# Kernel tuning notes

Hardware: AMD Instinct MI355X
Metric: run time of the kernel (lower is better)

Reference implementation:

```python
import jax, jax.numpy as jnp
import numpy as np


def log_g(x):
    # log of g(x) = where(x>=0, x+0.5, sigmoid(x)), computed stably in log space
    return jnp.where(x >= 0, jnp.log(jax.nn.relu(x) + 0.5), -jax.nn.softplus(-x))


def setup_inputs() -> dict:
    key = jax.random.key(0)
    k1, k2 = jax.random.split(key)
    B, S, D = 4, 4096, 1024
    x = jax.random.normal(k1, (B, S, D), dtype=jnp.float32)
    W_hg = jax.random.normal(k2, (2 * D, D), dtype=jnp.float32) * (1.0 / np.sqrt(D))
    return {"x": x, "W_hg": W_hg}


def reference(x, W_hg):
    # x: [B, S, D], W_hg: [2D, D]
    hg = jnp.einsum('bsd,ed->bse', x, W_hg)  # [B, S, 2D]
    hidden, gate = jnp.split(hg, 2, axis=-1)

    log_coeffs = -jax.nn.softplus(gate)       # log(1 - z)
    log_z = -jax.nn.softplus(-gate)            # log(z)
    log_values = log_z + log_g(hidden)

    # Heinsen associative scan in log space along seq axis
    a_star = jnp.cumsum(log_coeffs, axis=1)
    log_h0_plus_b_star = jax.lax.cumlogsumexp(log_values - a_star, axis=1)
    log_h = a_star + log_h0_plus_b_star
    out = jnp.exp(log_h)  # [B, S, D]; to_out is Identity (expansion_factor=1.0)
    return out
```

## Files before the change

### kernel.cpp

```cpp
#include <hip/hip_runtime.h>
#include <stdint.h>

#define B_ 4
#define S_ 4096
#define D_ 1024
#define E_ 2048
#define K_ 1024
#define M_ (B_*S_)
#define SEG 64
#define NSEG (S_/SEG)

typedef __bf16 bf16x8 __attribute__((ext_vector_type(8)));
typedef float  f32x4  __attribute__((ext_vector_type(4)));
typedef _Float16 f16x2 __attribute__((ext_vector_type(2)));

__device__ __forceinline__ unsigned short f2bf(float f) {
    union { float f; unsigned int u; } x; x.f = f;
    unsigned int u = x.u;
    return (unsigned short)((u + 0x7fffu + ((u >> 16) & 1u)) >> 16);
}

__device__ __forceinline__ void gload16(const void* g, void* l) {
    __builtin_amdgcn_global_load_lds(
        (const __attribute__((address_space(1))) void*)(uintptr_t)g,
        (__attribute__((address_space(3))) void*)(uintptr_t)l,
        16, 0, 0);
}

__device__ __forceinline__ unsigned int packCV(float hid, float gat) {
    float e  = __expf(gat);
    float c  = __builtin_amdgcn_rcpf(1.f + e);
    float gg = (hid >= 0.f) ? (hid + 0.5f)
                            : __builtin_amdgcn_rcpf(1.f + __expf(-hid));
    float v  = (1.f - c) * gg;
    union { f16x2 h; unsigned int u; } pk;
    pk.h[0] = (_Float16)c; pk.h[1] = (_Float16)v;
    return pk.u;
}

__global__ void cvt_x(const float* __restrict__ x, unsigned short* __restrict__ xb, int n) {
    int i = (blockIdx.x * blockDim.x + threadIdx.x) * 4;
    if (i >= n) return;
    float4 f = *(const float4*)(x + i);
    ushort4 o;
    o.x = f2bf(f.x); o.y = f2bf(f.y); o.z = f2bf(f.z); o.w = f2bf(f.w);
    *(ushort4*)(xb + i) = o;
}

__global__ void cvt_w(const float* __restrict__ w, unsigned short* __restrict__ wb) {
    int i = (blockIdx.x * blockDim.x + threadIdx.x) * 4;
    int r = i >> 10;
    int k = i & 1023;
    int d = r >> 1, g = r & 1;
    const float* src = w + (size_t)(g * D_ + d) * K_ + k;
    float4 f = *(const float4*)src;
    ushort4 o;
    o.x = f2bf(f.x); o.y = f2bf(f.y); o.z = f2bf(f.z); o.w = f2bf(f.w);
    *(ushort4*)(wb + i) = o;
}

#define BM 128
#define BN 128
#define BK 32

__global__ __launch_bounds__(256, 2)
void gemm_ep(const unsigned short* __restrict__ xb,
             const unsigned short* __restrict__ wb,
             unsigned int* __restrict__ cv,
             float2* __restrict__ segCV) {
    __shared__ unsigned short As[BM * BK];
    __shared__ unsigned short Bs[BN * BK];
    __shared__ __align__(16) unsigned int Ep[4][64][36];

    const int tid  = threadIdx.x;
    const int lane = tid & 63;
    const int w    = tid >> 6;
    const int mBase = blockIdx.y * BM;
    const int eBase = blockIdx.x * BN;
    const int waveM = (w >> 1) * 64;
    const int waveN = (w & 1) * 64;

    f32x4 acc[4][4] = {};

    const int row0 = tid >> 2, cu = tid & 3;
    const unsigned short* aG0 = xb + (size_t)(mBase + row0) * K_ + cu * 8;
    const unsigned short* aG1 = aG0 + (size_t)64 * K_;
    const unsigned short* bG0 = wb + (size_t)(eBase + row0) * K_ + cu * 8;
    const unsigned short* bG1 = bG0 + (size_t)64 * K_;
    unsigned short* aL0 = As + (size_t)(w * 64) * 8;
    unsigned short* aL1 = As + (size_t)(256 + w * 64) * 8;
    unsigned short* bL0 = Bs + (size_t)(w * 64) * 8;
    unsigned short* bL1 = Bs + (size_t)(256 + w * 64) * 8;

    const int mrow = lane & 15;
    const int kg   = (lane >> 4) * 8;

    for (int k0 = 0; k0 < K_; k0 += BK) {
        __syncthreads();
        gload16(aG0 + k0, aL0);
        gload16(aG1 + k0, aL1);
        gload16(bG0 + k0, bL0);
        gload16(bG1 + k0, bL1);
        __syncthreads();

        bf16x8 af[4], bfr[4];
#pragma unroll
        for (int i = 0; i < 4; i++)
            af[i] = *(const bf16x8*)(As + (size_t)(waveM + i * 16 + mrow) * BK + kg);
#pragma unroll
        for (int j = 0; j < 4; j++)
            bfr[j] = *(const bf16x8*)(Bs + (size_t)(waveN + j * 16 + mrow) * BK + kg);
#pragma unroll
        for (int i = 0; i < 4; i++)
#pragma unroll
            for (int j = 0; j < 4; j++)
                acc[i][j] = __builtin_amdgcn_mfma_f32_16x16x32_bf16(af[i], bfr[j], acc[i][j], 0, 0, 0);
    }

    const int q    = lane >> 4;
    const int odd  = lane & 1;
    const int colL = (lane & 15) >> 1;
    unsigned int* EpW = &Ep[w][0][0];

#pragma unroll
    for (int i = 0; i < 4; i++) {
#pragma unroll
        for (int j = 0; j < 4; j++) {
            float o0 = __shfl_xor(acc[i][j][0], 1, 64);
            float o1 = __shfl_xor(acc[i][j][1], 1, 64);
            float o2 = __shfl_xor(acc[i][j][2], 1, 64);
            float o3 = __shfl_xor(acc[i][j][3], 1, 64);
            float m0 = odd ? acc[i][j][2] : acc[i][j][0];
            float m1 = odd ? acc[i][j][3] : acc[i][j][1];
            float p0 = odd ? o2 : o0;
            float p1 = odd ? o3 : o1;
            float h0 = odd ? p0 : m0, g0 = odd ? m0 : p0;
            float h1 = odd ? p1 : m1, g1 = odd ? m1 : p1;
            int row = i * 16 + q * 4 + odd * 2;
            int col = j * 8 + colL;
            EpW[(row    ) * 36 + col] = packCV(h0, g0);
            EpW[(row + 1) * 36 + col] = packCV(h1, g1);
        }
    }
    const int srow = lane >> 3;
    const int schk = lane & 7;
    const size_t dBaseS = (size_t)((eBase + waveN) >> 1) + schk * 4;
#pragma unroll
    for (int gph = 0; gph < 8; gph++) {
        int row = gph * 8 + srow;
        uint4 valq = *(const uint4*)&EpW[row * 36 + schk * 4];
        size_t m = (size_t)(mBase + waveM + row);
        *(uint4*)(cv + m * D_ + dBaseS) = valq;
    }

    __syncthreads();
    float* scratch = (float*)As;

    {
        const int dl = tid & 63;
        const int qt = tid >> 6;
        const int wq = (qt >> 1) * 2 + (dl >> 5);
        const int rBase = (qt & 1) * 32;
        const int c = dl & 31;
        const unsigned int* src = &Ep[wq][rBase][c];
        float C = 1.f, V = 0.f;
#pragma unroll 8
        for (int rr = 0; rr < 32; rr++) {
            union { unsigned int u; f16x2 h; } uu;
            uu.u = src[rr * 36];
            float cc = (float)uu.h[0], vv = (float)uu.h[1];
            V = fmaf(cc, V, vv);
            C *= cc;
        }
        scratch[(qt * 64 + dl) * 2 + 0] = C;
        scratch[(qt * 64 + dl) * 2 + 1] = V;
    }
    __syncthreads();
    if (tid < 128) {
        const int k  = tid >> 6;
        const int dl = tid & 63;
        float C0 = scratch[((2 * k    ) * 64 + dl) * 2 + 0];
        float V0 = scratch[((2 * k    ) * 64 + dl) * 2 + 1];
        float C1 = scratch[((2 * k + 1) * 64 + dl) * 2 + 0];
        float V1 = scratch[((2 * k + 1) * 64 + dl) * 2 + 1];
        int bj = blockIdx.y * 2 + k;
        int dg = blockIdx.x * 64 + dl;
        segCV[(size_t)bj * D_ + dg] = make_float2(C0 * C1, fmaf(C1, V0, V1));
    }
}

__global__ void scan_apply(const uint2* __restrict__ cv2,
                           const float2* __restrict__ segCV,
                           float2* __restrict__ out2) {
    const int bj = blockIdx.x;
    const int jFirst = bj & ~(NSEG - 1);
    const int p = blockIdx.y * 256 + threadIdx.x;

    float h0 = 0.f, h1 = 0.f;
    const float4* sc4 = (const float4*)segCV;
    for (int j = jFirst; j < bj; j++) {
        float4 s = sc4[(size_t)j * (D_ / 2) + p];
        h0 = fmaf(s.x, h0, s.y);
        h1 = fmaf(s.z, h1, s.w);
    }

    size_t base = (size_t)bj * SEG * (D_ / 2) + p;
#pragma unroll 4
    for (int s = 0; s < SEG; s++) {
        uint2 u = cv2[base + (size_t)s * (D_ / 2)];
        union { unsigned int u; f16x2 h; } a, b; a.u = u.x; b.u = u.y;
        h0 = fmaf((float)a.h[0], h0, (float)a.h[1]);
        h1 = fmaf((float)b.h[0], h1, (float)b.h[1]);
        out2[base + (size_t)s * (D_ / 2)] = make_float2(h0, h1);
    }
}

extern "C" void kernel_launch(void* const* d_in, const int* in_sizes, int n_in,
                              void* d_out, int out_size, void* d_ws, size_t ws_size,
                              hipStream_t stream) {
    const float* x = (const float*)d_in[0];
    const float* wmat = (const float*)d_in[1];
    float* out = (float*)d_out;
    char* ws = (char*)d_ws;

    unsigned short* xb = (unsigned short*)(ws);
    unsigned short* wb = (unsigned short*)(ws + (32u << 20));
    unsigned int*   cv = (unsigned int*)(ws + (36u << 20));
    float2*      segCV = (float2*)(ws + (100u << 20));

    cvt_x<<<(M_ * K_) / 1024, 256, 0, stream>>>(x, xb, M_ * K_);
    cvt_w<<<(E_ * K_) / 1024, 256, 0, stream>>>(wmat, wb);

    dim3 gg(E_ / BN, M_ / BM);
    gemm_ep<<<gg, 256, 0, stream>>>(xb, wb, cv, segCV);

    dim3 ga(B_ * NSEG, D_ / 512);
    scan_apply<<<ga, 256, 0, stream>>>((const uint2*)cv, (const float2*)segCV,
                                       (float2*)out);
}
```

Baseline: 239.7 us.

## Merge convert kernels, XCD-aware GEMM tile mapping, split segment scan from apply

Fuses the x and W bf16 conversions into one launch. Remaps GEMM block indices so each XCD handles a contiguous group of M tiles with 8x8 windows, aiming for better L2 reuse of A and B tiles. Replaces the quadratic per-block prefix over segment summaries with a separate small seg_scan kernel that writes each segment's carry-in state, so the apply kernel loads one value instead of looping over prior segments. Loads and stores in the apply kernel are batched by eight to raise memory-level parallelism. This adds one extra launch and a serial 64-step scan per channel.

```diff
diff --git a/kernel.cpp b/kernel.cpp
--- a/kernel.cpp
+++ b/kernel.cpp
@@ -38,25 +38,26 @@
     return pk.u;
 }
 
-__global__ void cvt_x(const float* __restrict__ x, unsigned short* __restrict__ xb, int n) {
-    int i = (blockIdx.x * blockDim.x + threadIdx.x) * 4;
-    if (i >= n) return;
-    float4 f = *(const float4*)(x + i);
-    ushort4 o;
-    o.x = f2bf(f.x); o.y = f2bf(f.y); o.z = f2bf(f.z); o.w = f2bf(f.w);
-    *(ushort4*)(xb + i) = o;
-}
-
-__global__ void cvt_w(const float* __restrict__ w, unsigned short* __restrict__ wb) {
-    int i = (blockIdx.x * blockDim.x + threadIdx.x) * 4;
-    int r = i >> 10;
-    int k = i & 1023;
-    int d = r >> 1, g = r & 1;
-    const float* src = w + (size_t)(g * D_ + d) * K_ + k;
-    float4 f = *(const float4*)src;
-    ushort4 o;
-    o.x = f2bf(f.x); o.y = f2bf(f.y); o.z = f2bf(f.z); o.w = f2bf(f.w);
-    *(ushort4*)(wb + i) = o;
+__global__ void cvt_xw(const float* __restrict__ x, unsigned short* __restrict__ xb,
+                       const float* __restrict__ w, unsigned short* __restrict__ wb) {
+    int b = blockIdx.x;
+    if (b < 16384) {
+        int i = (b * 256 + threadIdx.x) * 4;
+        float4 f = *(const float4*)(x + i);
+        ushort4 o;
+        o.x = f2bf(f.x); o.y = f2bf(f.y); o.z = f2bf(f.z); o.w = f2bf(f.w);
+        *(ushort4*)(xb + i) = o;
+    } else {
+        int i = ((b - 16384) * 256 + threadIdx.x) * 4;
+        int r = i >> 10;
+        int k = i & 1023;
+        int d = r >> 1, g = r & 1;
+        const float* src = w + (size_t)(g * D_ + d) * K_ + k;
+        float4 f = *(const float4*)src;
+        ushort4 o;
+        o.x = f2bf(f.x); o.y = f2bf(f.y); o.z = f2bf(f.z); o.w = f2bf(f.w);
+        *(ushort4*)(wb + i) = o;
+    }
 }
 
 #define BM 128
@@ -72,11 +73,19 @@
     __shared__ unsigned short Bs[BN * BK];
     __shared__ __align__(16) unsigned int Ep[4][64][36];
 
+    const int l    = blockIdx.x;
+    const int xcd  = l & 7;
+    const int r    = l >> 3;
+    const int sub  = r >> 6;
+    const int win  = r & 63;
+    const int eB   = (sub & 1) * 8 + (win & 7);
+    const int mB   = xcd * 16 + (sub >> 1) * 8 + (win >> 3);
+    const int mBase = mB * BM;
+    const int eBase = eB * BN;
+
     const int tid  = threadIdx.x;
     const int lane = tid & 63;
     const int w    = tid >> 6;
-    const int mBase = blockIdx.y * BM;
-    const int eBase = blockIdx.x * BN;
     const int waveM = (w >> 1) * 64;
     const int waveN = (w & 1) * 64;
 
@@ -183,35 +192,53 @@
         float V0 = scratch[((2 * k    ) * 64 + dl) * 2 + 1];
         float C1 = scratch[((2 * k + 1) * 64 + dl) * 2 + 0];
         float V1 = scratch[((2 * k + 1) * 64 + dl) * 2 + 1];
-        int bj = blockIdx.y * 2 + k;
-        int dg = blockIdx.x * 64 + dl;
+        int bj = mB * 2 + k;
+        int dg = (eBase >> 1) + dl;
         segCV[(size_t)bj * D_ + dg] = make_float2(C0 * C1, fmaf(C1, V0, V1));
     }
 }
 
-__global__ void scan_apply(const uint2* __restrict__ cv2,
-                           const float2* __restrict__ segCV,
-                           float2* __restrict__ out2) {
+__global__ void seg_scan(const float2* __restrict__ segCV, float* __restrict__ segH) {
+    int b = blockIdx.x;
+    int d = blockIdx.y * 256 + threadIdx.x;
+    float h = 0.f;
+    for (int j0 = 0; j0 < NSEG; j0 += 8) {
+        float2 s[8];
+#pragma unroll
+        for (int t = 0; t < 8; t++)
+            s[t] = segCV[(size_t)(b * NSEG + j0 + t) * D_ + d];
+#pragma unroll
+        for (int t = 0; t < 8; t++) {
+            segH[(size_t)(b * NSEG + j0 + t) * D_ + d] = h;
+            h = fmaf(s[t].x, h, s[t].y);
+        }
+    }
+}
+
+__global__ void seg_apply(const uint2* __restrict__ cv2,
+                          const float2* __restrict__ segH2, float2* __restrict__ out2) {
     const int bj = blockIdx.x;
-    const int jFirst = bj & ~(NSEG - 1);
-    const int p = blockIdx.y * 256 + threadIdx.x;
-
-    float h0 = 0.f, h1 = 0.f;
-    const float4* sc4 = (const float4*)segCV;
-    for (int j = jFirst; j < bj; j++) {
-        float4 s = sc4[(size_t)j * (D_ / 2) + p];
-        h0 = fmaf(s.x, h0, s.y);
-        h1 = fmaf(s.z, h1, s.w);
-    }
-
+    const int p  = blockIdx.y * 256 + threadIdx.x;
+
+    float2 hs = segH2[(size_t)bj * (D_ / 2) + p];
+    float h0 = hs.x, h1 = hs.y;
     size_t base = (size_t)bj * SEG * (D_ / 2) + p;
-#pragma unroll 4
-    for (int s = 0; s < SEG; s++) {
-        uint2 u = cv2[base + (size_t)s * (D_ / 2)];
-        union { unsigned int u; f16x2 h; } a, b; a.u = u.x; b.u = u.y;
-        h0 = fmaf((float)a.h[0], h0, (float)a.h[1]);
-        h1 = fmaf((float)b.h[0], h1, (float)b.h[1]);
-        out2[base + (size_t)s * (D_ / 2)] = make_float2(h0, h1);
+    for (int s0 = 0; s0 < SEG; s0 += 8) {
+        uint2 u[8];
+#pragma unroll
+        for (int t = 0; t < 8; t++)
+            u[t] = cv2[base + (size_t)(s0 + t) * (D_ / 2)];
+        float2 o[8];
+#pragma unroll
+        for (int t = 0; t < 8; t++) {
+            union { unsigned int u; f16x2 h; } a, b; a.u = u[t].x; b.u = u[t].y;
+            h0 = fmaf((float)a.h[0], h0, (float)a.h[1]);
+            h1 = fmaf((float)b.h[0], h1, (float)b.h[1]);
+            o[t] = make_float2(h0, h1);
+        }
+#pragma unroll
+        for (int t = 0; t < 8; t++)
+            out2[base + (size_t)(s0 + t) * (D_ / 2)] = o[t];
     }
 }
 
@@ -227,14 +254,16 @@
     unsigned short* wb = (unsigned short*)(ws + (32u << 20));
     unsigned int*   cv = (unsigned int*)(ws + (36u << 20));
     float2*      segCV = (float2*)(ws + (100u << 20));
-
-    cvt_x<<<(M_ * K_) / 1024, 256, 0, stream>>>(x, xb, M_ * K_);
-    cvt_w<<<(E_ * K_) / 1024, 256, 0, stream>>>(wmat, wb);
-
-    dim3 gg(E_ / BN, M_ / BM);
-    gemm_ep<<<gg, 256, 0, stream>>>(xb, wb, cv, segCV);
+    float*        segH = (float*)(ws + (102u << 20));
+
+    cvt_xw<<<18432, 256, 0, stream>>>(x, xb, wmat, wb);
+
+    gemm_ep<<<2048, 256, 0, stream>>>(xb, wb, cv, segCV);
+
+    dim3 gs(B_, D_ / 256);
+    seg_scan<<<gs, 256, 0, stream>>>((const float2*)segCV, segH);
 
     dim3 ga(B_ * NSEG, D_ / 512);
-    scan_apply<<<ga, 256, 0, stream>>>((const uint2*)cv, (const float2*)segCV,
-                                       (float2*)out);
-}
+    seg_apply<<<ga, 256, 0, stream>>>((const uint2*)cv, (const float2*)segH,
+                                      (float2*)out);
+}
```

New measurement: 233.5 us. -2.6%, faster.
